# Optimization experiments

Hardware: AMD Instinct MI355X
Metric: run time of the kernel (lower is better)

The kernel has to match this reference:

```python
import jax, jax.numpy as jnp
import numpy as np

SMOOTH = 1e-05


def _central_diff(x, axis):
    # Equivalent to conv3d with a 3x3x3 kernel having -1/+1 on `axis`,
    # zero padding=1: out[i] = x[i+1] - x[i-1] with zeros outside.
    pad = [(0, 0)] * x.ndim
    pad[axis] = (1, 1)
    xp = jnp.pad(x, pad)
    n = x.shape[axis]
    fwd = jax.lax.slice_in_dim(xp, 2, n + 2, axis=axis)
    bwd = jax.lax.slice_in_dim(xp, 0, n, axis=axis)
    return fwd - bwd


def _boundary(x):
    # x: [B, 1, D, H, W] -> soft boundary magnitude
    gx = _central_diff(x, 2)
    gy = _central_diff(x, 3)
    gz = _central_diff(x, 4)
    return jnp.sqrt(gx * gx + gy * gy + gz * gz + SMOOTH)


def setup_inputs() -> dict:
    key = jax.random.key(0)
    k1, k2 = jax.random.split(key)
    shape = (2, 1, 192, 192, 192)
    pred = jax.random.uniform(k1, shape, dtype=jnp.float32)
    target = jax.random.uniform(k2, shape, dtype=jnp.float32)
    return {"pred": pred, "target": target}


def reference(pred, target):
    pb = _boundary(pred)
    tb = _boundary(target)
    intersection = jnp.sum(pb * tb)
    dice = (2.0 * intersection + SMOOTH) / (jnp.sum(pb) + jnp.sum(tb) + SMOOTH)
    return 1.0 - dice
```

## Files before the change

### kernel.cpp

```cpp
#include <hip/hip_runtime.h>

constexpr int DSZ = 192, HSZ = 192, WSZ = 192, BSZ = 2;
constexpr int WQ  = WSZ / 4;
constexpr int HT  = 12;
constexpr int NHT = HSZ / HT;
constexpr int DT  = 12;
constexpr int NDC = DSZ / DT;
constexpr int TPB = 192;
constexpr int NBLOCKS = BSZ * NHT * NDC;
constexpr int PPT = HT * WQ / TPB;
constexpr int HW  = HSZ * WSZ;
constexpr float SMOOTH = 1e-5f;

__device__ __forceinline__ float4 ld4(const float* __restrict__ p) {
    return *reinterpret_cast<const float4*>(p);
}

__device__ __forceinline__ float fsqrt(float x) {
    return __builtin_amdgcn_sqrtf(x);
}

__device__ __forceinline__ void mag4(float4 c, float4 hm, float4 hn,
                                     float4 d0, float4 d1, float wl, float wr,
                                     float o[4]) {
    float gx0 = d1.x - d0.x, gx1 = d1.y - d0.y, gx2 = d1.z - d0.z, gx3 = d1.w - d0.w;
    float gy0 = hn.x - hm.x, gy1 = hn.y - hm.y, gy2 = hn.z - hm.z, gy3 = hn.w - hm.w;
    float gz0 = c.y - wl,    gz1 = c.z - c.x,   gz2 = c.w - c.y,   gz3 = wr - c.z;
    o[0] = fsqrt(fmaf(gx0, gx0, fmaf(gy0, gy0, fmaf(gz0, gz0, SMOOTH))));
    o[1] = fsqrt(fmaf(gx1, gx1, fmaf(gy1, gy1, fmaf(gz1, gz1, SMOOTH))));
    o[2] = fsqrt(fmaf(gx2, gx2, fmaf(gy2, gy2, fmaf(gz2, gz2, SMOOTH))));
    o[3] = fsqrt(fmaf(gx3, gx3, fmaf(gy3, gy3, fmaf(gz3, gz3, SMOOTH))));
}

__device__ __forceinline__ void edges(float4 r, int wq, float& wl, float& wr) {
    float up = __shfl_up(r.w, 1);
    float dn = __shfl_down(r.x, 1);
    wl = (wq > 0)      ? up : 0.f;
    wr = (wq < WQ - 1) ? dn : 0.f;
}

__global__ __launch_bounds__(TPB)
void bl_main(const float* __restrict__ pred,
             const float* __restrict__ target,
             double* __restrict__ acc) {
    __shared__ float4 sbuf[2][2][HT + 2][WQ];

    const int bid = (int)blockIdx.x;
    const int swz = (bid & 7) * (NBLOCKS / 8) + (bid >> 3);
    int t = swz;
    const int dc = t % NDC; t /= NDC;
    const int ht = t % NHT; t /= NHT;
    const int b  = t;
    const int d0 = dc * DT;
    const int h0 = ht * HT;

    const int tid = threadIdx.x;
    const int wq  = tid % WQ;
    const int r0  = tid / WQ;

    const float4 z = make_float4(0.f, 0.f, 0.f, 0.f);
    const float* __restrict__ base0 = pred   + (size_t)b * DSZ * HW + (size_t)h0 * WSZ + wq * 4;
    const float* __restrict__ base1 = target + (size_t)b * DSZ * HW + (size_t)h0 * WSZ + wq * 4;
    const float* base[2] = { base0, base1 };

    const bool isHalo = (tid < 2 * WQ);
    const int  hrow   = (tid < WQ) ? -1 : HT;
    const int  hwq    = (tid < WQ) ? tid : tid - WQ;
    const bool hvalid = isHalo && (h0 + hrow >= 0) && (h0 + hrow < HSZ);
    const float* hbase[2] = {
        pred   + (size_t)b * DSZ * HW + (size_t)(h0 + hrow) * WSZ + hwq * 4,
        target + (size_t)b * DSZ * HW + (size_t)(h0 + hrow) * WSZ + hwq * 4 };

    float4 cP[PPT][2], cC[PPT][2], cN[PPT][2], gN[PPT][2];
    float4 hNxt[2], gH[2];

    #pragma unroll
    for (int k = 0; k < PPT; ++k) {
        const size_t ro = (size_t)(r0 + 4 * k) * WSZ;
        #pragma unroll
        for (int a = 0; a < 2; ++a) {
            cP[k][a] = (d0 > 0) ? ld4(base[a] + ro + (size_t)(d0 - 1) * HW) : z;
            cC[k][a] = ld4(base[a] + ro + (size_t)d0 * HW);
            cN[k][a] = ld4(base[a] + ro + (size_t)(d0 + 1) * HW);
        }
    }
    float4 hCur[2];
    #pragma unroll
    for (int a = 0; a < 2; ++a) {
        hCur[a] = hvalid ? ld4(hbase[a] + (size_t)d0 * HW)       : z;
        hNxt[a] = hvalid ? ld4(hbase[a] + (size_t)(d0 + 1) * HW) : z;
    }
    #pragma unroll
    for (int k = 0; k < PPT; ++k)
        #pragma unroll
        for (int a = 0; a < 2; ++a)
            sbuf[0][a][r0 + 4 * k + 1][wq] = cC[k][a];
    if (isHalo) {
        #pragma unroll
        for (int a = 0; a < 2; ++a)
            sbuf[0][a][hrow + 1][hwq] = hCur[a];
    }
    __syncthreads();

    float s_pt = 0.f, s_p = 0.f, s_t = 0.f;

    #pragma unroll 1
    for (int s = 0; s < DT; ++s) {
        const int cur = s & 1, nxt = cur ^ 1;
        const int q = d0 + s + 2;
        const bool vq = (q < DSZ);

        #pragma unroll
        for (int k = 0; k < PPT; ++k) {
            const size_t ro = (size_t)(r0 + 4 * k) * WSZ + (size_t)q * HW;
            #pragma unroll
            for (int a = 0; a < 2; ++a)
                gN[k][a] = vq ? ld4(base[a] + ro) : z;
        }
        #pragma unroll
        for (int a = 0; a < 2; ++a)
            gH[a] = (vq && hvalid) ? ld4(hbase[a] + (size_t)q * HW) : z;

        #pragma unroll
        for (int k = 0; k < PPT; ++k) {
            const int r = r0 + 4 * k;
            float m[2][4];
            #pragma unroll
            for (int a = 0; a < 2; ++a) {
                float4 hm = sbuf[cur][a][r][wq];
                float4 hn = sbuf[cur][a][r + 2][wq];
                float wl, wr;
                edges(cC[k][a], wq, wl, wr);
                mag4(cC[k][a], hm, hn, cP[k][a], cN[k][a], wl, wr, m[a]);
            }
            #pragma unroll
            for (int j = 0; j < 4; ++j) {
                s_pt = fmaf(m[0][j], m[1][j], s_pt);
                s_p += m[0][j];
                s_t += m[1][j];
            }
        }

        #pragma unroll
        for (int k = 0; k < PPT; ++k)
            #pragma unroll
            for (int a = 0; a < 2; ++a)
                sbuf[nxt][a][r0 + 4 * k + 1][wq] = cN[k][a];
        if (isHalo) {
            #pragma unroll
            for (int a = 0; a < 2; ++a)
                sbuf[nxt][a][hrow + 1][hwq] = hNxt[a];
        }

        #pragma unroll
        for (int k = 0; k < PPT; ++k)
            #pragma unroll
            for (int a = 0; a < 2; ++a) {
                cP[k][a] = cC[k][a];
                cC[k][a] = cN[k][a];
                cN[k][a] = gN[k][a];
            }
        hNxt[0] = gH[0]; hNxt[1] = gH[1];
        __syncthreads();
    }

    #pragma unroll
    for (int off = 32; off; off >>= 1) {
        s_pt += __shfl_down(s_pt, off);
        s_p  += __shfl_down(s_p,  off);
        s_t  += __shfl_down(s_t,  off);
    }

    __shared__ float red[3][4];
    const int lane = tid & 63;
    const int wid  = tid >> 6;
    if (lane == 0) {
        red[wid][0] = s_pt;
        red[wid][1] = s_p;
        red[wid][2] = s_t;
    }
    __syncthreads();
    if (tid == 0) {
        double a_pt = 0.0, a_p = 0.0, a_t = 0.0;
        #pragma unroll
        for (int k = 0; k < 3; ++k) {
            a_pt += (double)red[k][0];
            a_p  += (double)red[k][1];
            a_t  += (double)red[k][2];
        }
        atomicAdd(&acc[0],  a_pt);
        atomicAdd(&acc[8],  a_p);
        atomicAdd(&acc[16], a_t);
    }
}

__global__ void bl_final(const double* __restrict__ acc, float* __restrict__ out) {
    const double I = acc[0];
    const double Pm = acc[8];
    const double Tm = acc[16];
    const double dice = (2.0 * I + 1e-5) / (Pm + Tm + 1e-5);
    out[0] = (float)(1.0 - dice);
}

extern "C" void kernel_launch(void* const* d_in, const int* in_sizes, int n_in,
                              void* d_out, int out_size, void* d_ws, size_t ws_size,
                              hipStream_t stream) {
    const float* pred   = (const float*)d_in[0];
    const float* target = (const float*)d_in[1];
    double* acc = (double*)d_ws;

    (void)hipMemsetAsync(d_ws, 0, 17 * sizeof(double), stream);
    bl_main<<<NBLOCKS, TPB, 0, stream>>>(pred, target, acc);
    bl_final<<<1, 1, 0, stream>>>(acc, (float*)d_out);
}
```

Baseline: 36.99 us.

## Deepen global-load prefetch to two planes and use a lighter LDS-only barrier

The depth-streaming loop now prefetches two D-planes ahead instead of one, using ping-pong register buffers, and unrolls the loop by two so the buffer roles stay static. The workgroup barrier is replaced by a custom one that waits only on LDS counters, letting outstanding global loads remain in flight across the barrier. The aim is to hide global memory latency better, at the cost of more registers per thread and a hand-written barrier that depends on correct waitcnt semantics.

Result: slower. 50.07 us (+35.3%).

```diff
diff --git a/kernel.cpp b/kernel.cpp
--- a/kernel.cpp
+++ b/kernel.cpp
@@ -20,6 +20,12 @@
     return __builtin_amdgcn_sqrtf(x);
 }
 
+__device__ __forceinline__ void wg_barrier() {
+    asm volatile("s_waitcnt lgkmcnt(0)" ::: "memory");
+    __builtin_amdgcn_s_barrier();
+    __builtin_amdgcn_sched_barrier(0);
+}
+
 __device__ __forceinline__ void mag4(float4 c, float4 hm, float4 hn,
                                      float4 d0, float4 d1, float wl, float wr,
                                      float o[4]) {
@@ -39,6 +45,61 @@
     wr = (wq < WQ - 1) ? dn : 0.f;
 }
 
+#define BL_STEP(S, CUR, NXT, GI, GC, HI, HC)                                   \
+    {                                                                          \
+        const int q   = d0 + (S) + 3;                                          \
+        const bool vq = ((S) <= DT - 3) && (q < DSZ);                          \
+        _Pragma("unroll")                                                      \
+        for (int k = 0; k < PPT; ++k) {                                        \
+            const size_t ro = (size_t)(r0 + 4 * k) * WSZ + (size_t)q * HW;     \
+            GI[k][0] = vq ? ld4(base0 + ro) : z;                               \
+            GI[k][1] = vq ? ld4(base1 + ro) : z;                               \
+        }                                                                      \
+        HI[0] = (vq && hvalid) ? ld4(hbase0 + (size_t)q * HW) : z;             \
+        HI[1] = (vq && hvalid) ? ld4(hbase1 + (size_t)q * HW) : z;             \
+        _Pragma("unroll")                                                      \
+        for (int k = 0; k < PPT; ++k) {                                        \
+            const int r = r0 + 4 * k;                                          \
+            float m0[4], m1[4];                                                \
+            {                                                                  \
+                float4 hm = sbuf[CUR][0][r][wq];                               \
+                float4 hn = sbuf[CUR][0][r + 2][wq];                           \
+                float wl, wr;                                                  \
+                edges(cC[k][0], wq, wl, wr);                                   \
+                mag4(cC[k][0], hm, hn, cP[k][0], cN[k][0], wl, wr, m0);        \
+            }                                                                  \
+            {                                                                  \
+                float4 hm = sbuf[CUR][1][r][wq];                               \
+                float4 hn = sbuf[CUR][1][r + 2][wq];                           \
+                float wl, wr;                                                  \
+                edges(cC[k][1], wq, wl, wr);                                   \
+                mag4(cC[k][1], hm, hn, cP[k][1], cN[k][1], wl, wr, m1);        \
+            }                                                                  \
+            _Pragma("unroll")                                                  \
+            for (int j = 0; j < 4; ++j) {                                      \
+                s_pt = fmaf(m0[j], m1[j], s_pt);                               \
+                s_p += m0[j];                                                  \
+                s_t += m1[j];                                                  \
+            }                                                                  \
+        }                                                                      \
+        _Pragma("unroll")                                                      \
+        for (int k = 0; k < PPT; ++k) {                                        \
+            sbuf[NXT][0][r0 + 4 * k + 1][wq] = cN[k][0];                       \
+            sbuf[NXT][1][r0 + 4 * k + 1][wq] = cN[k][1];                       \
+        }                                                                      \
+        if (isHalo) {                                                          \
+            sbuf[NXT][0][hrow + 1][hwq] = hNxt[0];                             \
+            sbuf[NXT][1][hrow + 1][hwq] = hNxt[1];                             \
+        }                                                                      \
+        _Pragma("unroll")                                                      \
+        for (int k = 0; k < PPT; ++k) {                                        \
+            cP[k][0] = cC[k][0]; cC[k][0] = cN[k][0]; cN[k][0] = GC[k][0];     \
+            cP[k][1] = cC[k][1]; cC[k][1] = cN[k][1]; cN[k][1] = GC[k][1];     \
+        }                                                                      \
+        hNxt[0] = HC[0]; hNxt[1] = HC[1];                                      \
+        wg_barrier();                                                          \
+    }
+
 __global__ __launch_bounds__(TPB)
 void bl_main(const float* __restrict__ pred,
              const float* __restrict__ target,
@@ -61,34 +122,39 @@
     const float4 z = make_float4(0.f, 0.f, 0.f, 0.f);
     const float* __restrict__ base0 = pred   + (size_t)b * DSZ * HW + (size_t)h0 * WSZ + wq * 4;
     const float* __restrict__ base1 = target + (size_t)b * DSZ * HW + (size_t)h0 * WSZ + wq * 4;
-    const float* base[2] = { base0, base1 };
 
     const bool isHalo = (tid < 2 * WQ);
     const int  hrow   = (tid < WQ) ? -1 : HT;
     const int  hwq    = (tid < WQ) ? tid : tid - WQ;
     const bool hvalid = isHalo && (h0 + hrow >= 0) && (h0 + hrow < HSZ);
-    const float* hbase[2] = {
-        pred   + (size_t)b * DSZ * HW + (size_t)(h0 + hrow) * WSZ + hwq * 4,
-        target + (size_t)b * DSZ * HW + (size_t)(h0 + hrow) * WSZ + hwq * 4 };
-
-    float4 cP[PPT][2], cC[PPT][2], cN[PPT][2], gN[PPT][2];
-    float4 hNxt[2], gH[2];
+    const float* __restrict__ hbase0 =
+        pred   + (size_t)b * DSZ * HW + (size_t)(h0 + hrow) * WSZ + hwq * 4;
+    const float* __restrict__ hbase1 =
+        target + (size_t)b * DSZ * HW + (size_t)(h0 + hrow) * WSZ + hwq * 4;
+
+    float4 cP[PPT][2], cC[PPT][2], cN[PPT][2];
+    float4 fA[PPT][2], fB[PPT][2];
+    float4 hNxt[2], hA[2], hB[2];
 
     #pragma unroll
     for (int k = 0; k < PPT; ++k) {
         const size_t ro = (size_t)(r0 + 4 * k) * WSZ;
         #pragma unroll
         for (int a = 0; a < 2; ++a) {
-            cP[k][a] = (d0 > 0) ? ld4(base[a] + ro + (size_t)(d0 - 1) * HW) : z;
-            cC[k][a] = ld4(base[a] + ro + (size_t)d0 * HW);
-            cN[k][a] = ld4(base[a] + ro + (size_t)(d0 + 1) * HW);
+            const float* bb = a ? base1 : base0;
+            cP[k][a] = (d0 > 0) ? ld4(bb + ro + (size_t)(d0 - 1) * HW) : z;
+            cC[k][a] = ld4(bb + ro + (size_t)d0 * HW);
+            cN[k][a] = ld4(bb + ro + (size_t)(d0 + 1) * HW);
+            fA[k][a] = ld4(bb + ro + (size_t)(d0 + 2) * HW);
         }
     }
     float4 hCur[2];
     #pragma unroll
     for (int a = 0; a < 2; ++a) {
-        hCur[a] = hvalid ? ld4(hbase[a] + (size_t)d0 * HW)       : z;
-        hNxt[a] = hvalid ? ld4(hbase[a] + (size_t)(d0 + 1) * HW) : z;
+        const float* hb = a ? hbase1 : hbase0;
+        hCur[a] = hvalid ? ld4(hb + (size_t)d0 * HW)       : z;
+        hNxt[a] = hvalid ? ld4(hb + (size_t)(d0 + 1) * HW) : z;
+        hA[a]   = hvalid ? ld4(hb + (size_t)(d0 + 2) * HW) : z;
     }
     #pragma unroll
     for (int k = 0; k < PPT; ++k)
@@ -100,68 +166,15 @@
         for (int a = 0; a < 2; ++a)
             sbuf[0][a][hrow + 1][hwq] = hCur[a];
     }
-    __syncthreads();
+    wg_barrier();
 
     float s_pt = 0.f, s_p = 0.f, s_t = 0.f;
 
     #pragma unroll 1
-    for (int s = 0; s < DT; ++s) {
-        const int cur = s & 1, nxt = cur ^ 1;
-        const int q = d0 + s + 2;
-        const bool vq = (q < DSZ);
-
-        #pragma unroll
-        for (int k = 0; k < PPT; ++k) {
-            const size_t ro = (size_t)(r0 + 4 * k) * WSZ + (size_t)q * HW;
-            #pragma unroll
-            for (int a = 0; a < 2; ++a)
-                gN[k][a] = vq ? ld4(base[a] + ro) : z;
-        }
-        #pragma unroll
-        for (int a = 0; a < 2; ++a)
-            gH[a] = (vq && hvalid) ? ld4(hbase[a] + (size_t)q * HW) : z;
-
-        #pragma unroll
-        for (int k = 0; k < PPT; ++k) {
-            const int r = r0 + 4 * k;
-            float m[2][4];
-            #pragma unroll
-            for (int a = 0; a < 2; ++a) {
-                float4 hm = sbuf[cur][a][r][wq];
-                float4 hn = sbuf[cur][a][r + 2][wq];
-                float wl, wr;
-                edges(cC[k][a], wq, wl, wr);
-                mag4(cC[k][a], hm, hn, cP[k][a], cN[k][a], wl, wr, m[a]);
-            }
-            #pragma unroll
-            for (int j = 0; j < 4; ++j) {
-                s_pt = fmaf(m[0][j], m[1][j], s_pt);
-                s_p += m[0][j];
-                s_t += m[1][j];
-            }
-        }
-
-        #pragma unroll
-        for (int k = 0; k < PPT; ++k)
-            #pragma unroll
-            for (int a = 0; a < 2; ++a)
-                sbuf[nxt][a][r0 + 4 * k + 1][wq] = cN[k][a];
-        if (isHalo) {
-            #pragma unroll
-            for (int a = 0; a < 2; ++a)
-                sbuf[nxt][a][hrow + 1][hwq] = hNxt[a];
-        }
-
-        #pragma unroll
-        for (int k = 0; k < PPT; ++k)
-            #pragma unroll
-            for (int a = 0; a < 2; ++a) {
-                cP[k][a] = cC[k][a];
-                cC[k][a] = cN[k][a];
-                cN[k][a] = gN[k][a];
-            }
-        hNxt[0] = gH[0]; hNxt[1] = gH[1];
-        __syncthreads();
+    for (int u = 0; u < DT / 2; ++u) {
+        const int s0 = 2 * u;
+        BL_STEP(s0,     0, 1, fB, fA, hB, hA)
+        BL_STEP(s0 + 1, 1, 0, fA, fB, hA, hB)
     }
 
     #pragma unroll
```
